# Optimization experiments

Hardware: AMD Instinct MI355X
Metric: run time of the kernel (lower is better)

## Reference

```python
import jax, jax.numpy as jnp
import numpy as np

BN_EPS = 1e-5

def _bn(x, g, b):
    # BatchNorm1d, training-mode batch statistics
    mu = x.mean(axis=0)
    var = x.var(axis=0)
    return g * (x - mu) / jnp.sqrt(var + BN_EPS) + b

def setup_inputs() -> dict:
    key = jax.random.key(0)
    ks = jax.random.split(key, 10)
    B2, D_in, D1, DIMS, C = 16384, 1024, 512, 256, 40
    B = B2 // 2
    def w(k, shape, fan_in):
        return jax.random.normal(k, shape, jnp.float32) / np.float32(np.sqrt(fan_in))
    return {
        "lufeat": jax.random.normal(ks[0], (B2, D_in), jnp.float32),
        "llabel": jax.random.randint(ks[1], (B,), 0, C),
        "W1": w(ks[2], (D_in, D1), D_in), "b1": jnp.zeros(D1, jnp.float32),
        "W2": w(ks[3], (D1, DIMS), D1), "b2": jnp.zeros(DIMS, jnp.float32),
        "W3": w(ks[4], (DIMS + C, 256), DIMS + C), "b3": jnp.zeros(256, jnp.float32),
        "W4": w(ks[5], (256, 64), 256), "b4": jnp.zeros(64, jnp.float32),
        "W5": w(ks[6], (64, 1), 64), "b5": jnp.zeros(1, jnp.float32),
        "g1": jnp.ones(256, jnp.float32), "be1": jnp.zeros(256, jnp.float32),
        "g2": jnp.ones(64, jnp.float32), "be2": jnp.zeros(64, jnp.float32),
        "mbank0": jax.random.normal(ks[7], (C, DIMS), jnp.float32),
        "start0": jnp.zeros(C, jnp.float32),
    }

def reference(lufeat, llabel, W1, b1, W2, b2, W3, b3, W4, b4, W5, b5,
              g1, be1, g2, be2, mbank0, start0):
    B = lufeat.shape[0] // 2
    h = (lufeat @ W1 + b1) @ W2 + b2            # [2B, dims]
    h = h / jnp.linalg.norm(h, axis=1, keepdims=True)
    lfeat, ufeat = h[:B], h[B:]

    # Sequential per-sample memory-bank scatter/EMA update (detached feats)
    lf_sg = jax.lax.stop_gradient(lfeat)
    def step(carry, xs):
        start, mbank = carry
        lab, feat = xs
        row = jnp.where(start[lab] == 0, feat, 0.9 * mbank[lab] + 0.1 * feat)
        return (start.at[lab].set(1.0), mbank.at[lab].set(row)), None
    (_, mbank), _ = jax.lax.scan(step, (start0, mbank0), (llabel, lf_sg))
    mbank = jax.lax.stop_gradient(mbank)

    # cdist retrieval: [B, C] euclidean distances
    lm = jnp.linalg.norm(lfeat[:, None, :] - mbank[None, :, :], axis=-1)
    lscores = lm.min(axis=-1)
    um = jnp.linalg.norm(ufeat[:, None, :] - mbank[None, :, :], axis=-1)

    uf = jnp.concatenate([ufeat, um], axis=-1)   # [B, dims + C]
    u = jax.nn.relu(_bn(uf @ W3 + b3, g1, be1))
    u = jax.nn.relu(_bn(u @ W4 + b4, g2, be2))   # dropout = identity (eval)
    uscores = u @ W5 + b5                        # [B, 1]
    return lscores, uscores, mbank
```

## Files before the change

kernel.cpp:

```cpp
#include <hip/hip_runtime.h>
#include <hip/hip_bf16.h>
#include <stdint.h>

typedef __attribute__((ext_vector_type(4))) float f32x4;
typedef __attribute__((ext_vector_type(8))) short s16x8;
typedef __attribute__((ext_vector_type(4))) unsigned short u16x4;
typedef __attribute__((ext_vector_type(4))) int i32x4;

#define B2T 16384
#define BH 8192
#define DIN 1024
#define DD1 512
#define DIMS 256
#define NC 40
#define CAPS 2048

__device__ __forceinline__ unsigned short f2b(float f) {
  unsigned int u = __builtin_bit_cast(unsigned int, f);
  u += 0x7FFFu + ((u >> 16) & 1u);
  return (unsigned short)(u >> 16);
}

__device__ __forceinline__ float b2f(unsigned short u) {
  return __builtin_bit_cast(float, ((unsigned int)u) << 16);
}

__global__ __launch_bounds__(256) void prep_all(const float* __restrict__ W1,
                                                const float* __restrict__ W2,
                                                const float* __restrict__ b1,
                                                const float* __restrict__ b2,
                                                const float* __restrict__ W3,
                                                const float* __restrict__ W4,
                                                unsigned short* __restrict__ WeffT,
                                                float* __restrict__ beff,
                                                unsigned short* __restrict__ W3T,
                                                unsigned short* __restrict__ W4T,
                                                float* __restrict__ statz) {
  __shared__ float W1s[32][36];
  __shared__ float W2sT[32][36];
  int b = blockIdx.x, t = threadIdx.x;
  if (b < 256) {
    int k0 = (b & 31) * 32, n0 = (b >> 5) * 32;
    int nn = t & 31, kq = t >> 5;
    f32x4 acc = (f32x4){0.f, 0.f, 0.f, 0.f};
    for (int j0 = 0; j0 < DD1; j0 += 32) {
#pragma unroll
      for (int i = 0; i < 4; ++i) {
        int idx = t + 256 * i;
        int kk = idx >> 5, jj = idx & 31;
        W1s[kk][jj] = W1[(size_t)(k0 + kk) * DD1 + j0 + jj];
        W2sT[jj][kk] = W2[(size_t)(j0 + kk) * DIMS + n0 + jj];
      }
      __syncthreads();
#pragma unroll
      for (int jj4 = 0; jj4 < 8; ++jj4) {
        f32x4 w2 = *(const f32x4*)&W2sT[nn][jj4 * 4];
        f32x4 w1_0 = *(const f32x4*)&W1s[kq * 4 + 0][jj4 * 4];
        f32x4 w1_1 = *(const f32x4*)&W1s[kq * 4 + 1][jj4 * 4];
        f32x4 w1_2 = *(const f32x4*)&W1s[kq * 4 + 2][jj4 * 4];
        f32x4 w1_3 = *(const f32x4*)&W1s[kq * 4 + 3][jj4 * 4];
        acc[0] += w1_0[0] * w2[0] + w1_0[1] * w2[1] + w1_0[2] * w2[2] + w1_0[3] * w2[3];
        acc[1] += w1_1[0] * w2[0] + w1_1[1] * w2[1] + w1_1[2] * w2[2] + w1_1[3] * w2[3];
        acc[2] += w1_2[0] * w2[0] + w1_2[1] * w2[1] + w1_2[2] * w2[2] + w1_2[3] * w2[3];
        acc[3] += w1_3[0] * w2[0] + w1_3[1] * w2[1] + w1_3[2] * w2[2] + w1_3[3] * w2[3];
      }
      __syncthreads();
    }
    u16x4 pk = {f2b(acc[0]), f2b(acc[1]), f2b(acc[2]), f2b(acc[3])};
    *(u16x4*)(WeffT + (size_t)(n0 + nn) * DIN + k0 + kq * 4) = pk;
  } else if (b == 256) {
    float a0 = 0.f, a1 = 0.f, a2 = 0.f, a3 = 0.f, a4 = 0.f, a5 = 0.f, a6 = 0.f, a7 = 0.f;
    for (int j = 0; j < DD1; j += 8) {
      a0 += b1[j + 0] * W2[(size_t)(j + 0) * DIMS + t];
      a1 += b1[j + 1] * W2[(size_t)(j + 1) * DIMS + t];
      a2 += b1[j + 2] * W2[(size_t)(j + 2) * DIMS + t];
      a3 += b1[j + 3] * W2[(size_t)(j + 3) * DIMS + t];
      a4 += b1[j + 4] * W2[(size_t)(j + 4) * DIMS + t];
      a5 += b1[j + 5] * W2[(size_t)(j + 5) * DIMS + t];
      a6 += b1[j + 6] * W2[(size_t)(j + 6) * DIMS + t];
      a7 += b1[j + 7] * W2[(size_t)(j + 7) * DIMS + t];
    }
    beff[t] = b2[t] + (((a0 + a1) + (a2 + a3)) + ((a4 + a5) + (a6 + a7)));
  } else if (b < 577) {
    int idx = (b - 257) * 256 + t;
    int n = idx / 320, k = idx - n * 320;
    float v = (k < 296) ? W3[(size_t)k * 256 + n] : 0.0f;
    W3T[(size_t)n * 320 + k] = f2b(v);
  } else if (b < 641) {
    int idx = (b - 577) * 256 + t;
    int n = idx >> 8, k = idx & 255;
    W4T[(size_t)n * 256 + k] = f2b(W4[(size_t)k * 64 + n]);
  } else {
    for (int i = t; i < 640; i += 256) statz[i] = 0.0f;
  }
}

template <int AMODE, int NB, int MI, int CW, int EPI, int K, int TPB>
__global__ __launch_bounds__(TPB) void gemm_core(
    const void* __restrict__ Aptr, int lda, const unsigned short* __restrict__ BT,
    const float* __restrict__ bias, float* __restrict__ C, int ldc,
    float* __restrict__ sums, float* __restrict__ ssqs,
    const float* __restrict__ bnsum, const float* __restrict__ bnssq,
    const float* __restrict__ bng, const float* __restrict__ bnbe,
    unsigned short* __restrict__ uf) {
  constexpr int NW = TPB / 64;
  constexpr int RG = NW / CW;
  constexpr int AR = RG * MI * 16;
  constexpr int ACH = AR * 8;
  constexpr int ABN = (ACH + TPB - 1) / TPB;
  constexpr int BBN = NB * 8 / TPB;
  __shared__ short A_s[AR][72];
  __shared__ short B_s[NB][72];
  __shared__ float rs[CW][AR];
  __shared__ float bsc_s[(AMODE == 2) ? 256 : 1];
  __shared__ float bsh_s[(AMODE == 2) ? 256 : 1];
  int t = threadIdx.x;
  int m0 = blockIdx.x * AR;
  int w = t >> 6, lane = t & 63, q = lane >> 4, ln = lane & 15;
  f32x4 acc[MI][4];
#pragma unroll
  for (int mi = 0; mi < MI; ++mi)
#pragma unroll
    for (int ni = 0; ni < 4; ++ni) acc[mi][ni] = (f32x4){0.f, 0.f, 0.f, 0.f};

  f32x4 pa0[ABN][2], pa1[ABN][2];
  s16x8 pab0[ABN], pab1[ABN];
  s16x8 pb0[BBN], pb1[BBN];

  auto issue = [&](int kbase, f32x4 (&paX)[ABN][2], s16x8 (&pabX)[ABN], s16x8 (&pbX)[BBN]) {
    if (ACH >= TPB || t < ACH) {
#pragma unroll
      for (int i = 0; i < ABN; ++i) {
        int ch = t + TPB * i, row = ch >> 3, kp = (ch & 7) * 8;
        if constexpr (AMODE == 1) {
          const unsigned short* A = (const unsigned short*)Aptr;
          pabX[i] = *(const s16x8*)(A + (size_t)(m0 + row) * lda + kbase + kp);
        } else {
          const float* A = (const float*)Aptr;
          const f32x4* src = (const f32x4*)(A + (size_t)(m0 + row) * lda + kbase + kp);
          paX[i][0] = src[0];
          paX[i][1] = src[1];
        }
      }
    }
#pragma unroll
    for (int i = 0; i < BBN; ++i) {
      int ch = t + TPB * i, n = ch >> 3, kp = (ch & 7) * 8;
      pbX[i] = *(const s16x8*)(BT + (size_t)n * K + kbase + kp);
    }
  };

  auto stage = [&](int kk, f32x4 (&paX)[ABN][2], s16x8 (&pabX)[ABN], s16x8 (&pbX)[BBN]) {
    if (ACH >= TPB || t < ACH) {
#pragma unroll
      for (int i = 0; i < ABN; ++i) {
        int ch = t + TPB * i, row = ch >> 3, kp = (ch & 7) * 8;
        if constexpr (AMODE == 1) {
          *(s16x8*)&A_s[row][kp] = pabX[i];
        } else {
          f32x4 v0 = paX[i][0], v1 = paX[i][1];
          if constexpr (AMODE == 2) {
            float vv[8] = {v0[0], v0[1], v0[2], v0[3], v1[0], v1[1], v1[2], v1[3]};
#pragma unroll
            for (int j = 0; j < 8; ++j) {
              int f = kk + kp + j;
              vv[j] = fmaxf(vv[j] * bsc_s[f] + bsh_s[f], 0.0f);
            }
            v0 = (f32x4){vv[0], vv[1], vv[2], vv[3]};
            v1 = (f32x4){vv[4], vv[5], vv[6], vv[7]};
          }
          s16x8 p;
          p[0] = (short)f2b(v0[0]); p[1] = (short)f2b(v0[1]);
          p[2] = (short)f2b(v0[2]); p[3] = (short)f2b(v0[3]);
          p[4] = (short)f2b(v1[0]); p[5] = (short)f2b(v1[1]);
          p[6] = (short)f2b(v1[2]); p[7] = (short)f2b(v1[3]);
          *(s16x8*)&A_s[row][kp] = p;
        }
      }
    }
#pragma unroll
    for (int i = 0; i < BBN; ++i) {
      int ch = t + TPB * i, n = ch >> 3, kp = (ch & 7) * 8;
      *(s16x8*)&B_s[n][kp] = pbX[i];
    }
  };

  auto compute = [&]() {
#pragma unroll
    for (int k32 = 0; k32 < 64; k32 += 32) {
      s16x8 af[MI];
      int ab = (w / CW) * MI * 16;
#pragma unroll
      for (int mi = 0; mi < MI; ++mi)
        af[mi] = *(const s16x8*)&A_s[ab + mi * 16 + ln][k32 + q * 8];
      int nb0 = (w % CW) * 64;
#pragma unroll
      for (int ni = 0; ni < 4; ++ni) {
        s16x8 bfr = *(const s16x8*)&B_s[nb0 + ni * 16 + ln][k32 + q * 8];
#pragma unroll
        for (int mi = 0; mi < MI; ++mi)
          acc[mi][ni] = __builtin_amdgcn_mfma_f32_16x16x32_bf16(af[mi], bfr, acc[mi][ni], 0, 0, 0);
      }
    }
  };

  if constexpr (AMODE == 2) {
    if (t < 256) {
      float mu = bnsum[t] * (1.0f / 8192.0f);
      float var = bnssq[t] * (1.0f / 8192.0f) - mu * mu;
      float sc = bng[t] * rsqrtf(var + 1e-5f);
      bsc_s[t] = sc;
      bsh_s[t] = bnbe[t] - mu * sc;
    }
    __syncthreads();
  }

  const int nst = K >> 6;
  issue(0, pa0, pab0, pb0);
  if (nst > 1) issue(64, pa1, pab1, pb1);

  for (int s = 0; s < nst; s += 2) {
    stage(s << 6, pa0, pab0, pb0);
    __syncthreads();
    if (s + 2 < nst) issue((s + 2) << 6, pa0, pab0, pb0);
    compute();
    __syncthreads();
    if (s + 1 < nst) {
      stage((s + 1) << 6, pa1, pab1, pb1);
      __syncthreads();
      if (s + 3 < nst) issue((s + 3) << 6, pa1, pab1, pb1);
      compute();
      __syncthreads();
    }
  }

  float v[MI][4][4];
#pragma unroll
  for (int mi = 0; mi < MI; ++mi)
#pragma unroll
    for (int ni = 0; ni < 4; ++ni) {
      float bv = bias[(w % CW) * 64 + ni * 16 + ln];
#pragma unroll
      for (int r = 0; r < 4; ++r) v[mi][ni][r] = acc[mi][ni][r] + bv;
    }

  if constexpr (EPI == 1) {
    float p[MI][4];
#pragma unroll
    for (int mi = 0; mi < MI; ++mi)
#pragma unroll
      for (int r = 0; r < 4; ++r) {
        float s = v[mi][0][r] * v[mi][0][r] + v[mi][1][r] * v[mi][1][r] +
                  v[mi][2][r] * v[mi][2][r] + v[mi][3][r] * v[mi][3][r];
        s += __shfl_xor(s, 1); s += __shfl_xor(s, 2);
        s += __shfl_xor(s, 4); s += __shfl_xor(s, 8);
        p[mi][r] = s;
      }
    if (ln == 0) {
#pragma unroll
      for (int mi = 0; mi < MI; ++mi)
#pragma unroll
        for (int r = 0; r < 4; ++r)
          rs[w % CW][(w / CW) * MI * 16 + mi * 16 + q * 4 + r] = p[mi][r];
    }
    __syncthreads();
    if (t < AR) {
      float s = rs[0][t];
#pragma unroll
      for (int i = 1; i < CW; ++i) s += rs[i][t];
      rs[0][t] = rsqrtf(s);
    }
    __syncthreads();
#pragma unroll
    for (int mi = 0; mi < MI; ++mi)
#pragma unroll
      for (int r = 0; r < 4; ++r) {
        int ribf = (w / CW) * MI * 16 + mi * 16 + q * 4 + r;
        float inv = rs[0][ribf];
        int grow = m0 + ribf;
#pragma unroll
        for (int ni = 0; ni < 4; ++ni) {
          int col = (w % CW) * 64 + ni * 16 + ln;
          float nv = v[mi][ni][r] * inv;
          if (grow < BH)
            C[(size_t)grow * ldc + col] = nv;
          else
            uf[(size_t)(grow - BH) * 320 + col] = f2b(nv);
        }
      }
  } else {
#pragma unroll
    for (int mi = 0; mi < MI; ++mi)
#pragma unroll
      for (int ni = 0; ni < 4; ++ni)
#pragma unroll
        for (int r = 0; r < 4; ++r) {
          int grow = m0 + (w / CW) * MI * 16 + mi * 16 + q * 4 + r;
          int col = (w % CW) * 64 + ni * 16 + ln;
          C[(size_t)grow * ldc + col] = v[mi][ni][r];
        }
    if constexpr (EPI == 2 || EPI == 3) {
#pragma unroll
      for (int ni = 0; ni < 4; ++ni) {
        float s = 0.f, s2 = 0.f;
#pragma unroll
        for (int mi = 0; mi < MI; ++mi)
#pragma unroll
          for (int r = 0; r < 4; ++r) {
            float x = v[mi][ni][r];
            s += x; s2 += x * x;
          }
        s += __shfl_xor(s, 16); s += __shfl_xor(s, 32);
        s2 += __shfl_xor(s2, 16); s2 += __shfl_xor(s2, 32);
        if (q == 0) {
          int col = (w % CW) * 64 + ni * 16 + ln;
          atomicAdd(&sums[col], s);
          atomicAdd(&ssqs[col], s2);
        }
      }
    }
  }
}

__global__ __launch_bounds__(256) void bank_kernel(const int* __restrict__ llabel,
                                                   const float* __restrict__ Hn,
                                                   const float* __restrict__ mbank0,
                                                   const float* __restrict__ start0,
                                                   float* __restrict__ mbank_out,
                                                   float* __restrict__ msq) {
  __shared__ i32x4 lab4[BH / 4];
  __shared__ int idx_s[CAPS];
  __shared__ int wcnt[4];
  __shared__ float red[4];
  int t = threadIdx.x, c = blockIdx.x;
  int w = t >> 6, lane = t & 63;

  for (int i = t; i < BH / 4; i += 256) lab4[i] = ((const i32x4*)llabel)[i];
  __syncthreads();
  const int* lab_s = (const int*)lab4;

  int base0 = w * (BH / 4);
  int cnt = 0;
  for (int b = 0; b < BH / 4; b += 64)
    cnt += (int)__popcll(__ballot(lab_s[base0 + b + lane] == c));
  if (lane == 0) wcnt[w] = cnt;
  __syncthreads();
  int off = 0;
#pragma unroll
  for (int i = 0; i < 4; ++i)
    if (i < w) off += wcnt[i];
  int Ktot = wcnt[0] + wcnt[1] + wcnt[2] + wcnt[3];

  int running = off;
  for (int b = 0; b < BH / 4; b += 64) {
    bool hit = lab_s[base0 + b + lane] == c;
    unsigned long long mk = __ballot(hit);
    if (hit) {
      int pos = running + (int)__popcll(mk & ((1ull << lane) - 1ull));
      if (pos < CAPS) idx_s[pos] = base0 + b + lane;
    }
    running += (int)__popcll(mk);
  }
  __syncthreads();
  int K = Ktot < CAPS ? Ktot : CAPS;

  const float l09 = -0.15200309344504997f;
  bool fresh = (start0[c] == 0.0f);
  float out;
  if (K == 0) {
    out = mbank0[(size_t)c * DIMS + t];
  } else {
    float a0 = 0.f, a1 = 0.f, a2 = 0.f, a3 = 0.f, a4 = 0.f, a5 = 0.f, a6 = 0.f, a7 = 0.f;
    float w0fold = fresh ? exp2f((float)K * l09) : 0.f;
    int m = 0;
    for (; m + 8 <= K; m += 8) {
      float e = (float)(K - 1 - m);
      float wa = 0.1f * exp2f(e * l09) + (m == 0 ? w0fold : 0.f);
      a0 += wa * Hn[(size_t)idx_s[m + 0] * DIMS + t];
      a1 += 0.1f * exp2f((e - 1.f) * l09) * Hn[(size_t)idx_s[m + 1] * DIMS + t];
      a2 += 0.1f * exp2f((e - 2.f) * l09) * Hn[(size_t)idx_s[m + 2] * DIMS + t];
      a3 += 0.1f * exp2f((e - 3.f) * l09) * Hn[(size_t)idx_s[m + 3] * DIMS + t];
      a4 += 0.1f * exp2f((e - 4.f) * l09) * Hn[(size_t)idx_s[m + 4] * DIMS + t];
      a5 += 0.1f * exp2f((e - 5.f) * l09) * Hn[(size_t)idx_s[m + 5] * DIMS + t];
      a6 += 0.1f * exp2f((e - 6.f) * l09) * Hn[(size_t)idx_s[m + 6] * DIMS + t];
      a7 += 0.1f * exp2f((e - 7.f) * l09) * Hn[(size_t)idx_s[m + 7] * DIMS + t];
    }
    for (; m < K; ++m) {
      float wa = 0.1f * exp2f((float)(K - 1 - m) * l09) + (m == 0 ? w0fold : 0.f);
      a0 += wa * Hn[(size_t)idx_s[m] * DIMS + t];
    }
    float acc = ((a0 + a1) + (a2 + a3)) + ((a4 + a5) + (a6 + a7));
    float base_v = fresh ? 0.f : exp2f((float)K * l09) * mbank0[(size_t)c * DIMS + t];
    out = acc + base_v;
  }
  mbank_out[(size_t)c * DIMS + t] = out;
  float vv = out * out;
#pragma unroll
  for (int o = 32; o; o >>= 1) vv += __shfl_xor(vv, o);
  if ((t & 63) == 0) red[t >> 6] = vv;
  __syncthreads();
  if (t == 0) msq[c] = (red[0] + red[1]) + (red[2] + red[3]);
}

__global__ __launch_bounds__(256) void dist_kernel(const float* __restrict__ Hn,
                                                   const float* __restrict__ mbank,
                                                   const float* __restrict__ msq,
                                                   float* __restrict__ lscores,
                                                   unsigned short* __restrict__ uf) {
  __shared__ float Ms[NC][260];
  __shared__ float Hs[32][260];
  __shared__ float msq_s[NC];
  int t = threadIdx.x;
  int r0 = blockIdx.x * 32;
  for (int e = t; e < NC * 64; e += 256) {
    int i = e >> 6, d0 = (e & 63) * 4;
    *(f32x4*)&Ms[i][d0] = *(const f32x4*)(mbank + (size_t)i * DIMS + d0);
  }
  if (r0 < BH) {
    for (int e = t; e < 32 * 64; e += 256) {
      int i = e >> 6, d0 = (e & 63) * 4;
      *(f32x4*)&Hs[i][d0] = *(const f32x4*)(Hn + (size_t)(r0 + i) * DIMS + d0);
    }
  } else {
    for (int e = t; e < 32 * 32; e += 256) {
      int i = e >> 5, d0 = (e & 31) * 8;
      s16x8 vb = *(const s16x8*)(uf + (size_t)(r0 - BH + i) * 320 + d0);
#pragma unroll
      for (int j = 0; j < 8; ++j) Hs[i][d0 + j] = b2f((unsigned short)vb[j]);
    }
  }
  if (t < NC) msq_s[t] = msq[t];
  __syncthreads();
  int r = t >> 3, c0 = (t & 7) * 5;
  float g0 = 0, g1 = 0, g2 = 0, g3 = 0, g4 = 0;
  for (int d = 0; d < DIMS; d += 4) {
    f32x4 f = *(const f32x4*)&Hs[r][d];
    f32x4 m0v = *(const f32x4*)&Ms[c0 + 0][d];
    f32x4 m1v = *(const f32x4*)&Ms[c0 + 1][d];
    f32x4 m2v = *(const f32x4*)&Ms[c0 + 2][d];
    f32x4 m3v = *(const f32x4*)&Ms[c0 + 3][d];
    f32x4 m4v = *(const f32x4*)&Ms[c0 + 4][d];
    g0 += f[0] * m0v[0] + f[1] * m0v[1] + f[2] * m0v[2] + f[3] * m0v[3];
    g1 += f[0] * m1v[0] + f[1] * m1v[1] + f[2] * m1v[2] + f[3] * m1v[3];
    g2 += f[0] * m2v[0] + f[1] * m2v[1] + f[2] * m2v[2] + f[3] * m2v[3];
    g3 += f[0] * m3v[0] + f[1] * m3v[1] + f[2] * m3v[2] + f[3] * m3v[3];
    g4 += f[0] * m4v[0] + f[1] * m4v[1] + f[2] * m4v[2] + f[3] * m4v[3];
  }
  int row = r0 + r;
  float d2[5];
  d2[0] = 1.0f + msq_s[c0 + 0] - 2.0f * g0;
  d2[1] = 1.0f + msq_s[c0 + 1] - 2.0f * g1;
  d2[2] = 1.0f + msq_s[c0 + 2] - 2.0f * g2;
  d2[3] = 1.0f + msq_s[c0 + 3] - 2.0f * g3;
  d2[4] = 1.0f + msq_s[c0 + 4] - 2.0f * g4;
  if (row < BH) {
    float mn = fminf(fminf(fminf(d2[0], d2[1]), fminf(d2[2], d2[3])), d2[4]);
    mn = fminf(mn, __shfl_xor(mn, 1, 8));
    mn = fminf(mn, __shfl_xor(mn, 2, 8));
    mn = fminf(mn, __shfl_xor(mn, 4, 8));
    if ((t & 7) == 0) lscores[row] = sqrtf(fmaxf(mn, 0.0f));
  } else {
    unsigned short* dst = uf + (size_t)(row - BH) * 320 + 256 + c0;
#pragma unroll
    for (int qq = 0; qq < 5; ++qq) dst[qq] = f2b(sqrtf(fmaxf(d2[qq], 0.0f)));
  }
}

__global__ __launch_bounds__(256) void uscore_bn(const float* __restrict__ y2,
                                                 const float* __restrict__ sums2,
                                                 const float* __restrict__ ssqs2,
                                                 const float* __restrict__ g2,
                                                 const float* __restrict__ be2,
                                                 const float* __restrict__ W5,
                                                 const float* __restrict__ b5,
                                                 float* __restrict__ out) {
  int t = threadIdx.x;
  int wv = t >> 6, lane = t & 63;
  int row = blockIdx.x * 4 + wv;
  float mu = sums2[lane] * (1.0f / 8192.0f);
  float var = ssqs2[lane] * (1.0f / 8192.0f) - mu * mu;
  float sc = g2[lane] * rsqrtf(var + 1e-5f);
  float sh = be2[lane] - mu * sc;
  float v = fmaxf(y2[(size_t)row * 64 + lane] * sc + sh, 0.0f) * W5[lane];
#pragma unroll
  for (int o = 32; o; o >>= 1) v += __shfl_xor(v, o);
  if (lane == 0) out[row] = v + b5[0];
}

extern "C" void kernel_launch(void* const* d_in, const int* in_sizes, int n_in,
                              void* d_out, int out_size, void* d_ws, size_t ws_size,
                              hipStream_t stream) {
  const float* lufeat = (const float*)d_in[0];
  const int* llabel = (const int*)d_in[1];
  const float* W1 = (const float*)d_in[2];
  const float* b1 = (const float*)d_in[3];
  const float* W2 = (const float*)d_in[4];
  const float* b2 = (const float*)d_in[5];
  const float* W3 = (const float*)d_in[6];
  const float* b3 = (const float*)d_in[7];
  const float* W4 = (const float*)d_in[8];
  const float* b4 = (const float*)d_in[9];
  const float* W5 = (const float*)d_in[10];
  const float* b5 = (const float*)d_in[11];
  const float* g1 = (const float*)d_in[12];
  const float* be1 = (const float*)d_in[13];
  const float* g2 = (const float*)d_in[14];
  const float* be2 = (const float*)d_in[15];
  const float* mbank0 = (const float*)d_in[16];
  const float* start0 = (const float*)d_in[17];

  char* ws = (char*)d_ws;
  unsigned short* WeffT = (unsigned short*)(ws + 0);
  float* Hraw = (float*)(ws + 524288);
  float* ybuf = (float*)(ws + 524288);
  float* y2 = (float*)(ws + 8912896);
  unsigned short* uf = (unsigned short*)(ws + 17301504);
  unsigned short* W3T = (unsigned short*)(ws + 22544384);
  unsigned short* W4T = (unsigned short*)(ws + 22708224);
  float* beff = (float*)(ws + 22740992);
  float* sums1 = (float*)(ws + 22742016);
  float* ssq1 = sums1 + 256;
  float* sums2 = ssq1 + 256;
  float* ssq2 = sums2 + 64;
  float* msq = (float*)(ws + 22744576);

  float* lscores = (float*)d_out;
  float* uscores = lscores + 8192;
  float* mbank = uscores + 8192;

  prep_all<<<642, 256, 0, stream>>>(W1, W2, b1, b2, W3, W4, WeffT, beff, W3T, W4T, sums1);
  gemm_core<0, 256, 2, 4, 1, 1024, 256><<<512, 256, 0, stream>>>(
      lufeat, 1024, WeffT, beff, Hraw, 256,
      nullptr, nullptr, nullptr, nullptr, nullptr, nullptr, uf);
  bank_kernel<<<NC, 256, 0, stream>>>(llabel, Hraw, mbank0, start0, mbank, msq);
  dist_kernel<<<512, 256, 0, stream>>>(Hraw, mbank, msq, lscores, uf);
  gemm_core<1, 256, 1, 4, 2, 320, 512><<<256, 512, 0, stream>>>(
      uf, 320, W3T, b3, ybuf, 256,
      sums1, ssq1, nullptr, nullptr, nullptr, nullptr, nullptr);
  gemm_core<2, 64, 1, 1, 3, 256, 256><<<128, 256, 0, stream>>>(
      ybuf, 256, W4T, b4, y2, 64,
      sums2, ssq2, sums1, ssq1, g1, be1, nullptr);
  uscore_bn<<<2048, 256, 0, stream>>>(y2, sums2, ssq2, g2, be2, W5, b5, uscores);
}
```

Measured before the change: 238.1 us.

## Double-buffer GEMM LDS tiles and load B directly to LDS with swizzle

```diff
diff --git a/kernel.cpp b/kernel.cpp
--- a/kernel.cpp
+++ b/kernel.cpp
@@ -23,6 +23,12 @@
 
 __device__ __forceinline__ float b2f(unsigned short u) {
   return __builtin_bit_cast(float, ((unsigned int)u) << 16);
+}
+
+__device__ __forceinline__ void gload16(const void* g, void* l) {
+  __builtin_amdgcn_global_load_lds(
+      (const __attribute__((address_space(1))) void*)g,
+      (__attribute__((address_space(3))) void*)l, 16, 0, 0);
 }
 
 __global__ __launch_bounds__(256) void prep_all(const float* __restrict__ W1,
@@ -109,8 +115,9 @@
   constexpr int ACH = AR * 8;
   constexpr int ABN = (ACH + TPB - 1) / TPB;
   constexpr int BBN = NB * 8 / TPB;
-  __shared__ short A_s[AR][72];
-  __shared__ short B_s[NB][72];
+  constexpr int BBUF = NB * 128;
+  __shared__ __align__(16) short A_s[2][AR][72];
+  __shared__ __align__(16) char B_s[2 * BBUF];
   __shared__ float rs[CW][AR];
   __shared__ float bsc_s[(AMODE == 2) ? 256 : 1];
   __shared__ float bsh_s[(AMODE == 2) ? 256 : 1];
@@ -125,9 +132,8 @@
 
   f32x4 pa0[ABN][2], pa1[ABN][2];
   s16x8 pab0[ABN], pab1[ABN];
-  s16x8 pb0[BBN], pb1[BBN];
-
-  auto issue = [&](int kbase, f32x4 (&paX)[ABN][2], s16x8 (&pabX)[ABN], s16x8 (&pbX)[BBN]) {
+
+  auto issueA = [&](int kbase, f32x4 (&paX)[ABN][2], s16x8 (&pabX)[ABN]) {
     if (ACH >= TPB || t < ACH) {
 #pragma unroll
       for (int i = 0; i < ABN; ++i) {
@@ -143,20 +149,26 @@
         }
       }
     }
+  };
+
+  auto gloadB = [&](int kbase, int bufi) {
 #pragma unroll
     for (int i = 0; i < BBN; ++i) {
-      int ch = t + TPB * i, n = ch >> 3, kp = (ch & 7) * 8;
-      pbX[i] = *(const s16x8*)(BT + (size_t)n * K + kbase + kp);
+      int ch = t + TPB * i;
+      int n = ch >> 3, j = ch & 7;
+      int ksw = (j ^ (n & 7)) * 8;
+      gload16(BT + (size_t)n * K + kbase + ksw,
+              B_s + bufi * BBUF + (w * 64 + TPB * i) * 16);
     }
   };
 
-  auto stage = [&](int kk, f32x4 (&paX)[ABN][2], s16x8 (&pabX)[ABN], s16x8 (&pbX)[BBN]) {
+  auto stageA = [&](int kk, int bufi, f32x4 (&paX)[ABN][2], s16x8 (&pabX)[ABN]) {
     if (ACH >= TPB || t < ACH) {
 #pragma unroll
       for (int i = 0; i < ABN; ++i) {
         int ch = t + TPB * i, row = ch >> 3, kp = (ch & 7) * 8;
         if constexpr (AMODE == 1) {
-          *(s16x8*)&A_s[row][kp] = pabX[i];
+          *(s16x8*)&A_s[bufi][row][kp] = pabX[i];
         } else {
           f32x4 v0 = paX[i][0], v1 = paX[i][1];
           if constexpr (AMODE == 2) {
@@ -174,29 +186,26 @@
           p[2] = (short)f2b(v0[2]); p[3] = (short)f2b(v0[3]);
           p[4] = (short)f2b(v1[0]); p[5] = (short)f2b(v1[1]);
           p[6] = (short)f2b(v1[2]); p[7] = (short)f2b(v1[3]);
-          *(s16x8*)&A_s[row][kp] = p;
+          *(s16x8*)&A_s[bufi][row][kp] = p;
         }
       }
     }
-#pragma unroll
-    for (int i = 0; i < BBN; ++i) {
-      int ch = t + TPB * i, n = ch >> 3, kp = (ch & 7) * 8;
-      *(s16x8*)&B_s[n][kp] = pbX[i];
-    }
   };
 
-  auto compute = [&]() {
+  auto compute = [&](int cur) {
 #pragma unroll
     for (int k32 = 0; k32 < 64; k32 += 32) {
       s16x8 af[MI];
       int ab = (w / CW) * MI * 16;
 #pragma unroll
       for (int mi = 0; mi < MI; ++mi)
-        af[mi] = *(const s16x8*)&A_s[ab + mi * 16 + ln][k32 + q * 8];
+        af[mi] = *(const s16x8*)&A_s[cur][ab + mi * 16 + ln][k32 + q * 8];
       int nb0 = (w % CW) * 64;
 #pragma unroll
       for (int ni = 0; ni < 4; ++ni) {
-        s16x8 bfr = *(const s16x8*)&B_s[nb0 + ni * 16 + ln][k32 + q * 8];
+        int brow = nb0 + ni * 16 + ln;
+        int bb = (brow * 128 + (k32 + q * 8) * 2) ^ ((brow & 7) << 4);
+        s16x8 bfr = *(const s16x8*)(B_s + cur * BBUF + bb);
 #pragma unroll
         for (int mi = 0; mi < MI; ++mi)
           acc[mi][ni] = __builtin_amdgcn_mfma_f32_16x16x32_bf16(af[mi], bfr, acc[mi][ni], 0, 0, 0);
@@ -216,20 +225,23 @@
   }
 
   const int nst = K >> 6;
-  issue(0, pa0, pab0, pb0);
-  if (nst > 1) issue(64, pa1, pab1, pb1);
+  issueA(0, pa0, pab0);
+  gloadB(0, 0);
+  if (nst > 1) issueA(64, pa1, pab1);
+  stageA(0, 0, pa0, pab0);
+  __syncthreads();
 
   for (int s = 0; s < nst; s += 2) {
-    stage(s << 6, pa0, pab0, pb0);
-    __syncthreads();
-    if (s + 2 < nst) issue((s + 2) << 6, pa0, pab0, pb0);
-    compute();
+    if (s + 1 < nst) gloadB((s + 1) << 6, 1);
+    if (s + 2 < nst) issueA((s + 2) << 6, pa0, pab0);
+    compute(0);
+    if (s + 1 < nst) stageA((s + 1) << 6, 1, pa1, pab1);
     __syncthreads();
     if (s + 1 < nst) {
-      stage((s + 1) << 6, pa1, pab1, pb1);
-      __syncthreads();
-      if (s + 3 < nst) issue((s + 3) << 6, pa1, pab1, pb1);
-      compute();
+      if (s + 2 < nst) gloadB((s + 2) << 6, 0);
+      if (s + 3 < nst) issueA((s + 3) << 6, pa1, pab1);
+      compute(1);
+      if (s + 2 < nst) stageA((s + 2) << 6, 0, pa0, pab0);
       __syncthreads();
     }
   }
```

New measurement: 238.0 us. Within noise of the previous version (-0.1%).
